# Kernel tuning notes

Hardware: AMD Instinct MI355X
Metric: run time of the kernel (lower is better)

Reference implementation:

```python
import jax, jax.numpy as jnp
import numpy as np

B, F, V, K, D, H = 16384, 26, 100000, 16, 13, 400
IN_DIM = F * K + D  # 429
EPS = 1e-5


def _bn(x, g, b):
    # BatchNorm1d in training mode: batch statistics (biased var, like torch)
    m = jnp.mean(x, axis=0)
    v = jnp.mean((x - m) ** 2, axis=0)
    return g * (x - m) / jnp.sqrt(v + EPS) + b


def setup_inputs() -> dict:
    key = jax.random.key(0)
    ks = jax.random.split(key, 12)
    X_cat = jax.random.randint(ks[0], (B, F), 0, V)
    X_dense = jax.random.normal(ks[1], (B, D), dtype=jnp.float32)
    fm1_tables = jax.random.normal(ks[2], (F, V, 1), dtype=jnp.float32) * 0.01
    emb_tables = jax.random.normal(ks[3], (F, V, K), dtype=jnp.float32) * 0.01
    Wd = jax.random.normal(ks[4], (D, 1), dtype=jnp.float32) * 0.1
    bd = jnp.zeros((1,), jnp.float32)
    W1 = jax.random.normal(ks[5], (IN_DIM, H), dtype=jnp.float32) * (1.0 / np.sqrt(IN_DIM))
    b1 = jnp.zeros((H,), jnp.float32)
    g1 = jnp.ones((H,), jnp.float32)
    be1 = jnp.zeros((H,), jnp.float32)
    W2 = jax.random.normal(ks[6], (H, H), dtype=jnp.float32) * (1.0 / np.sqrt(H))
    b2 = jnp.zeros((H,), jnp.float32)
    g2 = jnp.ones((H,), jnp.float32)
    be2 = jnp.zeros((H,), jnp.float32)
    W3 = jax.random.normal(ks[7], (H, 1), dtype=jnp.float32) * (1.0 / np.sqrt(H))
    b3 = jnp.zeros((1,), jnp.float32)
    return dict(X_cat=X_cat, X_dense=X_dense, fm1_tables=fm1_tables,
                emb_tables=emb_tables, Wd=Wd, bd=bd, W1=W1, b1=b1, g1=g1,
                be1=be1, W2=W2, b2=b2, g2=g2, be2=be2, W3=W3, b3=b3)


def reference(X_cat, X_dense, fm1_tables, emb_tables, Wd, bd,
              W1, b1, g1, be1, W2, b2, g2, be2, W3, b3):
    gather = jax.vmap(lambda tab, idx: tab[idx], in_axes=(0, 1), out_axes=1)
    # 1st order: [B, F, 1] -> sum over fields -> [B, 1]
    y_1st = jnp.sum(gather(fm1_tables, X_cat), axis=1) + X_dense @ Wd + bd
    # 2nd order embeddings: [B, F, K]
    emb = gather(emb_tables, X_cat)
    s = jnp.sum(emb, axis=1)                 # [B, K]
    ix = s ** 2 - jnp.sum(emb ** 2, axis=1)  # [B, K]
    fm_y = 0.5 * jnp.sum(ix, axis=1, keepdims=True)
    # DNN on [flattened embeddings, dense]
    x = jnp.concatenate([emb.reshape(emb.shape[0], -1), X_dense], axis=1)
    h = jax.nn.relu(_bn(x @ W1 + b1, g1, be1))
    h = jax.nn.relu(_bn(h @ W2 + b2, g2, be2))
    dnn_y = h @ W3 + b3
    return y_1st + fm_y + dnn_y
```

## Files before the change

### kernel.cpp

```cpp
#include <hip/hip_runtime.h>
#include <stdint.h>

#define B_ROWS 16384
#define NF 26
#define NV 100000
#define ND 13
#define NH 400
#define XPAD 448
#define ZPAD 416
#define EPS 1e-5f

typedef __attribute__((ext_vector_type(8))) short short8;
typedef __attribute__((ext_vector_type(4))) float f32x4;
typedef __attribute__((ext_vector_type(4))) unsigned int uint4v;

__device__ inline float bf2f(unsigned short u) {
    union { unsigned int i; float f; } v; v.i = (unsigned int)u << 16; return v.f;
}
__device__ inline unsigned short f2bf(float f) {
    union { float f; unsigned int i; } v; v.f = f;
    unsigned int r = (v.i + 0x7fff + ((v.i >> 16) & 1)) >> 16;
    return (unsigned short)r;
}

#define X_OFF    0
#define Z1_OFF   14680064
#define W1S_OFF  28311552
#define W2S_OFF  28712960
#define BASE_OFF 29085696
#define ST_OFF   29151232

__global__ __launch_bounds__(256) void gather_prep(
    const int* __restrict__ Xcat, const float* __restrict__ Xdense,
    const float* __restrict__ fm1, const float* __restrict__ emb,
    const float* __restrict__ Wd, const float* __restrict__ bd,
    const float* __restrict__ W1, const float* __restrict__ W2,
    unsigned short* __restrict__ X, float* __restrict__ base,
    unsigned short* __restrict__ W1s, unsigned short* __restrict__ W2s,
    float* __restrict__ st)
{
    int tid = threadIdx.x;
    if (blockIdx.x >= 1024) {
        int c = (blockIdx.x - 1024) * 256 + tid;
        if (c < 256) {
            for (int i = tid; i < 1664; i += 256) st[i] = 0.f;
        }
        const float* W; unsigned short* dst; int K; int cc;
        if (c < 25088) { W = W1; dst = W1s; K = 429; cc = c; }
        else           { W = W2; dst = W2s; K = 400; cc = c - 25088; }
        int n  = cc % 448;
        int q  = (cc / 448) & 3;
        int kt = cc / 1792;
        unsigned short o[8];
        #pragma unroll
        for (int j = 0; j < 8; ++j) {
            int k = kt * 32 + q * 8 + j;
            float v = (n < NH && k < K) ? W[(size_t)k * NH + n] : 0.f;
            o[j] = f2bf(v);
        }
        *(uint4v*)(dst + (size_t)cc * 8) = *(uint4v*)o;
        return;
    }
    int r = blockIdx.x * 16 + (tid >> 4);
    int k = tid & 15;
    const int* idxp = Xcat + (size_t)r * NF;
    unsigned short* xrow = X + (size_t)r * XPAD;

    float s = 0.f, ss = 0.f;
    #pragma unroll
    for (int f = 0; f < NF; ++f) {
        int idx = idxp[f];
        float v = emb[((size_t)f * NV + idx) * 16 + k];
        s += v; ss += v * v;
        xrow[f * 16 + k] = f2bf(v);
    }
    float fmsum = fm1[(size_t)k * NV + idxp[k]];
    if (k < NF - 16) fmsum += fm1[(size_t)(k + 16) * NV + idxp[k + 16]];
    float dsum = 0.f;
    if (k < ND) {
        float xd = Xdense[(size_t)r * ND + k];
        dsum = xd * Wd[k];
        xrow[NF * 16 + k] = f2bf(xd);
    }
    xrow[429 + k] = 0;
    if (k < 3) xrow[445 + k] = 0;

    float ix = s * s - ss;
    float rf = fmsum, rd = dsum;
    #pragma unroll
    for (int off = 8; off; off >>= 1) {
        ix += __shfl_xor(ix, off, 16);
        rf += __shfl_xor(rf, off, 16);
        rd += __shfl_xor(rd, off, 16);
    }
    if (k == 0) base[r] = 0.5f * ix + rf + rd + bd[0];
}

template<int NT, int LDA, bool APPLY_BN>
__global__ __launch_bounds__(512, 2) void mfma_gemm(
    const unsigned short* __restrict__ A,
    const unsigned short* __restrict__ Wst,
    const float* __restrict__ bias,
    const float* __restrict__ gsumIn, const float* __restrict__ gsqIn,
    const float* __restrict__ g, const float* __restrict__ be,
    unsigned short* __restrict__ Z, int ldz,
    float* __restrict__ gsum, float* __restrict__ gsq)
{
    __shared__ unsigned short b_s[2][1792 * 8];
    __shared__ float sredS[4][416];
    __shared__ float sredQ[4][416];
    __shared__ float alpha_s[416], beta_s[416];

    const int tid = threadIdx.x;
    const int lane = tid & 63;
    const int wv = tid >> 6;
    const int rowgrp = wv & 3;
    const int nhalf = wv >> 2;
    const int l15 = lane & 15;
    const int qh = lane >> 4;
    const int m0 = blockIdx.x * 64;
    const int arow = m0 + rowgrp * 16 + l15;
    const int c0 = nhalf * 208;
    const int NFRAG = nhalf ? 12 : 13;

    if constexpr (APPLY_BN) {
        for (int c = tid; c < ZPAD; c += 512) {
            float a = 0.f, b = 0.f;
            if (c < NH) {
                float mean = gsumIn[c] * (1.f / B_ROWS);
                float var  = gsqIn[c] * (1.f / B_ROWS) - mean * mean;
                a = g[c] * rsqrtf(var + EPS);
                b = be[c] - mean * a;
            }
            alpha_s[c] = a; beta_s[c] = b;
        }
    }

    f32x4 acc[13];
    #pragma unroll
    for (int i = 0; i < 13; ++i) acc[i] = f32x4{0.f, 0.f, 0.f, 0.f};

    uint4v rg[4];
    #pragma unroll
    for (int i = 0; i < 4; ++i) {
        int c = i * 512 + tid;
        if (c < 1792) rg[i] = *(const uint4v*)(Wst + (size_t)c * 8);
    }
    short8 af_next = *(const short8*)(A + (size_t)arow * LDA + qh * 8);

    for (int kt = 0; kt < NT; ++kt) {
        __syncthreads();
        #pragma unroll
        for (int i = 0; i < 4; ++i) {
            int c = i * 512 + tid;
            if (c < 1792) *(uint4v*)(&b_s[kt & 1][(size_t)c * 8]) = rg[i];
        }
        if (kt + 1 < NT) {
            #pragma unroll
            for (int i = 0; i < 4; ++i) {
                int c = i * 512 + tid;
                if (c < 1792)
                    rg[i] = *(const uint4v*)(Wst + (size_t)(kt + 1) * 14336 + (size_t)c * 8);
            }
        }
        short8 af = af_next;
        if (kt + 1 < NT)
            af_next = *(const short8*)(A + (size_t)arow * LDA + (kt + 1) * 32 + qh * 8);

        if constexpr (APPLY_BN) {
            const int k0 = kt * 32 + qh * 8;
            #pragma unroll
            for (int j = 0; j < 8; ++j) {
                float f = bf2f((unsigned short)af[j]);
                f = fmaxf(0.f, alpha_s[k0 + j] * f + beta_s[k0 + j]);
                af[j] = (short)f2bf(f);
            }
        }
        __syncthreads();
        const unsigned short* bb = &b_s[kt & 1][(size_t)(qh * 448 + c0 + l15) * 8];
        #pragma unroll
        for (int nn = 0; nn < 13; ++nn) {
            if (nn < NFRAG) {
                short8 bf = *(const short8*)(bb + nn * 128);
                acc[nn] = __builtin_amdgcn_mfma_f32_16x16x32_bf16(af, bf, acc[nn], 0, 0, 0);
            }
        }
    }

    #pragma unroll
    for (int nn = 0; nn < 13; ++nn) {
        if (nn < NFRAG) {
            int col = c0 + nn * 16 + l15;
            float bv = bias[col];
            float ps = 0.f, pq = 0.f;
            #pragma unroll
            for (int q = 0; q < 4; ++q) {
                float v = acc[nn][q] + bv;
                ps += v; pq += v * v;
                Z[(size_t)(m0 + rowgrp * 16 + qh * 4 + q) * ldz + col] = f2bf(v);
            }
            ps += __shfl_xor(ps, 16, 64); ps += __shfl_xor(ps, 32, 64);
            pq += __shfl_xor(pq, 16, 64); pq += __shfl_xor(pq, 32, 64);
            if (lane < 16) { sredS[rowgrp][col] = ps; sredQ[rowgrp][col] = pq; }
        }
    }
    if (nhalf == 1) {
        int col = NH + l15;
        if (col < ldz) {
            #pragma unroll
            for (int q = 0; q < 4; ++q)
                Z[(size_t)(m0 + rowgrp * 16 + qh * 4 + q) * ldz + col] = 0;
        }
    }
    __syncthreads();
    for (int c = tid; c < NH; c += 512) {
        float s = sredS[0][c] + sredS[1][c] + sredS[2][c] + sredS[3][c];
        float q = sredQ[0][c] + sredQ[1][c] + sredQ[2][c] + sredQ[3][c];
        atomicAdd(&gsum[c], s);
        atomicAdd(&gsq[c], q);
    }
}

__global__ __launch_bounds__(256) void final_kernel(
    const unsigned short* __restrict__ Z2,
    const float* __restrict__ gsum2, const float* __restrict__ gsq2,
    const float* __restrict__ g2, const float* __restrict__ be2,
    const float* __restrict__ W3, const float* __restrict__ b3,
    const float* __restrict__ base, float* __restrict__ out)
{
    __shared__ float a2s[NH], b2s[NH], w3s[NH];
    int tid = threadIdx.x;
    for (int c = tid; c < NH; c += 256) {
        float mean = gsum2[c] * (1.f / B_ROWS);
        float var  = gsq2[c] * (1.f / B_ROWS) - mean * mean;
        float a = g2[c] * rsqrtf(var + EPS);
        a2s[c] = a;
        b2s[c] = be2[c] - mean * a;
        w3s[c] = W3[c];
    }
    __syncthreads();
    int lane = tid & 63;
    int wv = tid >> 6;
    bool act = lane < 50;
    int cb = lane * 8;
    float al[8], bb[8], w3[8];
    #pragma unroll
    for (int j = 0; j < 8; ++j) {
        al[j] = act ? a2s[cb + j] : 0.f;
        bb[j] = act ? b2s[cb + j] : 0.f;
        w3[j] = act ? w3s[cb + j] : 0.f;
    }
    int r0 = blockIdx.x * 32 + wv * 8;
    float bias3 = b3[0];
    for (int t = 0; t < 8; t += 2) {
        int r = r0 + t;
        float acc0 = 0.f, acc1 = 0.f;
        if (act) {
            short8 z0 = *(const short8*)(Z2 + (size_t)r * ZPAD + cb);
            short8 z1 = *(const short8*)(Z2 + (size_t)(r + 1) * ZPAD + cb);
            #pragma unroll
            for (int j = 0; j < 8; ++j) {
                acc0 += fmaxf(0.f, al[j] * bf2f((unsigned short)z0[j]) + bb[j]) * w3[j];
                acc1 += fmaxf(0.f, al[j] * bf2f((unsigned short)z1[j]) + bb[j]) * w3[j];
            }
        }
        #pragma unroll
        for (int off = 32; off; off >>= 1) {
            acc0 += __shfl_xor(acc0, off, 64);
            acc1 += __shfl_xor(acc1, off, 64);
        }
        if (lane == 0) out[r] = base[r] + acc0 + bias3;
        if (lane == 1) out[r + 1] = base[r + 1] + acc1 + bias3;
    }
}

extern "C" void kernel_launch(void* const* d_in, const int* in_sizes, int n_in,
                              void* d_out, int out_size, void* d_ws, size_t ws_size,
                              hipStream_t stream)
{
    const int*   Xcat = (const int*)d_in[0];
    const float* Xd   = (const float*)d_in[1];
    const float* fm1  = (const float*)d_in[2];
    const float* emb  = (const float*)d_in[3];
    const float* Wd   = (const float*)d_in[4];
    const float* bd   = (const float*)d_in[5];
    const float* W1   = (const float*)d_in[6];
    const float* b1   = (const float*)d_in[7];
    const float* g1   = (const float*)d_in[8];
    const float* be1  = (const float*)d_in[9];
    const float* W2   = (const float*)d_in[10];
    const float* b2   = (const float*)d_in[11];
    const float* g2   = (const float*)d_in[12];
    const float* be2  = (const float*)d_in[13];
    const float* W3   = (const float*)d_in[14];
    const float* b3   = (const float*)d_in[15];

    char* ws = (char*)d_ws;
    unsigned short* X   = (unsigned short*)(ws + X_OFF);
    unsigned short* Z1  = (unsigned short*)(ws + Z1_OFF);
    unsigned short* Z2  = X;
    unsigned short* W1s = (unsigned short*)(ws + W1S_OFF);
    unsigned short* W2s = (unsigned short*)(ws + W2S_OFF);
    float* base = (float*)(ws + BASE_OFF);
    float* st   = (float*)(ws + ST_OFF);
    float* gsum1 = st;          float* gsq1 = st + 416;
    float* gsum2 = st + 832;    float* gsq2 = st + 1248;
    float* out = (float*)d_out;

    gather_prep<<<1213, 256, 0, stream>>>(Xcat, Xd, fm1, emb, Wd, bd, W1, W2,
                                          X, base, W1s, W2s, st);

    mfma_gemm<14, XPAD, false><<<256, 512, 0, stream>>>(
        X, W1s, b1, nullptr, nullptr, nullptr, nullptr, Z1, ZPAD, gsum1, gsq1);

    mfma_gemm<13, ZPAD, true><<<256, 512, 0, stream>>>(
        Z1, W2s, b2, gsum1, gsq1, g1, be1, Z2, ZPAD, gsum2, gsq2);

    final_kernel<<<512, 256, 0, stream>>>(Z2, gsum2, gsq2, g2, be2, W3, b3, base, out);
}
```

Before: 83.89 us.

## Fuse gather, both GEMMs and head into one cooperative persistent kernel

Replaces four kernel launches with a single cooperative kernel of 256 blocks that uses grid-wide syncs between stages. The embedding gather now feeds the first GEMM's A operand straight from global tables into registers, so the bf16 X buffer is never materialized. The FM sums are accumulated during the GEMM K-loop. The aim is to remove launch gaps and the X write/read round-trip. In exchange it adds three grid barriers and gathers with less coalescing inside the GEMM loop, which may stall the MFMA pipeline. Occupancy is also limited to 256 blocks.

Measured after the change: 165.1 us. +96.8%, slower.

```diff
diff --git a/kernel.cpp b/kernel.cpp
--- a/kernel.cpp
+++ b/kernel.cpp
@@ -1,12 +1,12 @@
 #include <hip/hip_runtime.h>
+#include <hip/hip_cooperative_groups.h>
 #include <stdint.h>
 
+namespace cg = cooperative_groups;
+
 #define B_ROWS 16384
-#define NF 26
 #define NV 100000
-#define ND 13
 #define NH 400
-#define XPAD 448
 #define ZPAD 416
 #define EPS 1e-5f
 
@@ -23,169 +23,32 @@
     return (unsigned short)r;
 }
 
-#define X_OFF    0
-#define Z1_OFF   14680064
-#define W1S_OFF  28311552
-#define W2S_OFF  28712960
-#define BASE_OFF 29085696
-#define ST_OFF   29151232
-
-__global__ __launch_bounds__(256) void gather_prep(
-    const int* __restrict__ Xcat, const float* __restrict__ Xdense,
-    const float* __restrict__ fm1, const float* __restrict__ emb,
-    const float* __restrict__ Wd, const float* __restrict__ bd,
-    const float* __restrict__ W1, const float* __restrict__ W2,
-    unsigned short* __restrict__ X, float* __restrict__ base,
-    unsigned short* __restrict__ W1s, unsigned short* __restrict__ W2s,
-    float* __restrict__ st)
+#define Z1_OFF   0
+#define Z2_OFF   13631488
+#define W1S_OFF  26738688
+#define W2S_OFF  27140096
+#define BASE_OFF 27512832
+#define ST_OFF   27578368
+
+struct SmemPool {
+    unsigned short b_s[2][14336];
+    union {
+        struct { float S[4][416]; float Q[4][416]; } red;
+        struct { int xcat[1664]; float dense[1024]; float wd[16]; } gat;
+    } u;
+    float alpha_s[416], beta_s[416];
+};
+
+__device__ __forceinline__ void gemm_epilogue(
+    SmemPool& sm, f32x4* acc, int tid, int m0,
+    const float* __restrict__ bias, unsigned short* __restrict__ Z, int ldz,
+    bool padZ, float* __restrict__ gsum, float* __restrict__ gsq)
 {
-    int tid = threadIdx.x;
-    if (blockIdx.x >= 1024) {
-        int c = (blockIdx.x - 1024) * 256 + tid;
-        if (c < 256) {
-            for (int i = tid; i < 1664; i += 256) st[i] = 0.f;
-        }
-        const float* W; unsigned short* dst; int K; int cc;
-        if (c < 25088) { W = W1; dst = W1s; K = 429; cc = c; }
-        else           { W = W2; dst = W2s; K = 400; cc = c - 25088; }
-        int n  = cc % 448;
-        int q  = (cc / 448) & 3;
-        int kt = cc / 1792;
-        unsigned short o[8];
-        #pragma unroll
-        for (int j = 0; j < 8; ++j) {
-            int k = kt * 32 + q * 8 + j;
-            float v = (n < NH && k < K) ? W[(size_t)k * NH + n] : 0.f;
-            o[j] = f2bf(v);
-        }
-        *(uint4v*)(dst + (size_t)cc * 8) = *(uint4v*)o;
-        return;
-    }
-    int r = blockIdx.x * 16 + (tid >> 4);
-    int k = tid & 15;
-    const int* idxp = Xcat + (size_t)r * NF;
-    unsigned short* xrow = X + (size_t)r * XPAD;
-
-    float s = 0.f, ss = 0.f;
-    #pragma unroll
-    for (int f = 0; f < NF; ++f) {
-        int idx = idxp[f];
-        float v = emb[((size_t)f * NV + idx) * 16 + k];
-        s += v; ss += v * v;
-        xrow[f * 16 + k] = f2bf(v);
-    }
-    float fmsum = fm1[(size_t)k * NV + idxp[k]];
-    if (k < NF - 16) fmsum += fm1[(size_t)(k + 16) * NV + idxp[k + 16]];
-    float dsum = 0.f;
-    if (k < ND) {
-        float xd = Xdense[(size_t)r * ND + k];
-        dsum = xd * Wd[k];
-        xrow[NF * 16 + k] = f2bf(xd);
-    }
-    xrow[429 + k] = 0;
-    if (k < 3) xrow[445 + k] = 0;
-
-    float ix = s * s - ss;
-    float rf = fmsum, rd = dsum;
-    #pragma unroll
-    for (int off = 8; off; off >>= 1) {
-        ix += __shfl_xor(ix, off, 16);
-        rf += __shfl_xor(rf, off, 16);
-        rd += __shfl_xor(rd, off, 16);
-    }
-    if (k == 0) base[r] = 0.5f * ix + rf + rd + bd[0];
-}
-
-template<int NT, int LDA, bool APPLY_BN>
-__global__ __launch_bounds__(512, 2) void mfma_gemm(
-    const unsigned short* __restrict__ A,
-    const unsigned short* __restrict__ Wst,
-    const float* __restrict__ bias,
-    const float* __restrict__ gsumIn, const float* __restrict__ gsqIn,
-    const float* __restrict__ g, const float* __restrict__ be,
-    unsigned short* __restrict__ Z, int ldz,
-    float* __restrict__ gsum, float* __restrict__ gsq)
-{
-    __shared__ unsigned short b_s[2][1792 * 8];
-    __shared__ float sredS[4][416];
-    __shared__ float sredQ[4][416];
-    __shared__ float alpha_s[416], beta_s[416];
-
-    const int tid = threadIdx.x;
-    const int lane = tid & 63;
-    const int wv = tid >> 6;
-    const int rowgrp = wv & 3;
-    const int nhalf = wv >> 2;
-    const int l15 = lane & 15;
-    const int qh = lane >> 4;
-    const int m0 = blockIdx.x * 64;
-    const int arow = m0 + rowgrp * 16 + l15;
+    const int lane = tid & 63, wv = tid >> 6;
+    const int rowgrp = wv & 3, nhalf = wv >> 2;
+    const int l15 = lane & 15, qh = lane >> 4;
     const int c0 = nhalf * 208;
     const int NFRAG = nhalf ? 12 : 13;
-
-    if constexpr (APPLY_BN) {
-        for (int c = tid; c < ZPAD; c += 512) {
-            float a = 0.f, b = 0.f;
-            if (c < NH) {
-                float mean = gsumIn[c] * (1.f / B_ROWS);
-                float var  = gsqIn[c] * (1.f / B_ROWS) - mean * mean;
-                a = g[c] * rsqrtf(var + EPS);
-                b = be[c] - mean * a;
-            }
-            alpha_s[c] = a; beta_s[c] = b;
-        }
-    }
-
-    f32x4 acc[13];
-    #pragma unroll
-    for (int i = 0; i < 13; ++i) acc[i] = f32x4{0.f, 0.f, 0.f, 0.f};
-
-    uint4v rg[4];
-    #pragma unroll
-    for (int i = 0; i < 4; ++i) {
-        int c = i * 512 + tid;
-        if (c < 1792) rg[i] = *(const uint4v*)(Wst + (size_t)c * 8);
-    }
-    short8 af_next = *(const short8*)(A + (size_t)arow * LDA + qh * 8);
-
-    for (int kt = 0; kt < NT; ++kt) {
-        __syncthreads();
-        #pragma unroll
-        for (int i = 0; i < 4; ++i) {
-            int c = i * 512 + tid;
-            if (c < 1792) *(uint4v*)(&b_s[kt & 1][(size_t)c * 8]) = rg[i];
-        }
-        if (kt + 1 < NT) {
-            #pragma unroll
-            for (int i = 0; i < 4; ++i) {
-                int c = i * 512 + tid;
-                if (c < 1792)
-                    rg[i] = *(const uint4v*)(Wst + (size_t)(kt + 1) * 14336 + (size_t)c * 8);
-            }
-        }
-        short8 af = af_next;
-        if (kt + 1 < NT)
-            af_next = *(const short8*)(A + (size_t)arow * LDA + (kt + 1) * 32 + qh * 8);
-
-        if constexpr (APPLY_BN) {
-            const int k0 = kt * 32 + qh * 8;
-            #pragma unroll
-            for (int j = 0; j < 8; ++j) {
-                float f = bf2f((unsigned short)af[j]);
-                f = fmaxf(0.f, alpha_s[k0 + j] * f + beta_s[k0 + j]);
-                af[j] = (short)f2bf(f);
-            }
-        }
-        __syncthreads();
-        const unsigned short* bb = &b_s[kt & 1][(size_t)(qh * 448 + c0 + l15) * 8];
-        #pragma unroll
-        for (int nn = 0; nn < 13; ++nn) {
-            if (nn < NFRAG) {
-                short8 bf = *(const short8*)(bb + nn * 128);
-                acc[nn] = __builtin_amdgcn_mfma_f32_16x16x32_bf16(af, bf, acc[nn], 0, 0, 0);
-            }
-        }
-    }
 
     #pragma unroll
     for (int nn = 0; nn < 13; ++nn) {
@@ -201,10 +64,10 @@
             }
             ps += __shfl_xor(ps, 16, 64); ps += __shfl_xor(ps, 32, 64);
             pq += __shfl_xor(pq, 16, 64); pq += __shfl_xor(pq, 32, 64);
-            if (lane < 16) { sredS[rowgrp][col] = ps; sredQ[rowgrp][col] = pq; }
-        }
-    }
-    if (nhalf == 1) {
+            if (lane < 16) { sm.u.red.S[rowgrp][col] = ps; sm.u.red.Q[rowgrp][col] = pq; }
+        }
+    }
+    if (padZ && nhalf == 1) {
         int col = NH + l15;
         if (col < ldz) {
             #pragma unroll
@@ -214,63 +77,276 @@
     }
     __syncthreads();
     for (int c = tid; c < NH; c += 512) {
-        float s = sredS[0][c] + sredS[1][c] + sredS[2][c] + sredS[3][c];
-        float q = sredQ[0][c] + sredQ[1][c] + sredQ[2][c] + sredQ[3][c];
-        atomicAdd(&gsum[c], s);
-        atomicAdd(&gsq[c], q);
-    }
-}
-
-__global__ __launch_bounds__(256) void final_kernel(
-    const unsigned short* __restrict__ Z2,
-    const float* __restrict__ gsum2, const float* __restrict__ gsq2,
+        atomicAdd(&gsum[c], sm.u.red.S[0][c] + sm.u.red.S[1][c] + sm.u.red.S[2][c] + sm.u.red.S[3][c]);
+        atomicAdd(&gsq[c],  sm.u.red.Q[0][c] + sm.u.red.Q[1][c] + sm.u.red.Q[2][c] + sm.u.red.Q[3][c]);
+    }
+}
+
+__global__ __launch_bounds__(512, 4) void deepfm_mega(
+    const int* __restrict__ Xcat, const float* __restrict__ Xd,
+    const float* __restrict__ fm1, const float* __restrict__ emb,
+    const float* __restrict__ Wd, const float* __restrict__ bd,
+    const float* __restrict__ W1, const float* __restrict__ b1,
+    const float* __restrict__ g1, const float* __restrict__ be1,
+    const float* __restrict__ W2, const float* __restrict__ b2,
     const float* __restrict__ g2, const float* __restrict__ be2,
     const float* __restrict__ W3, const float* __restrict__ b3,
-    const float* __restrict__ base, float* __restrict__ out)
+    unsigned short* __restrict__ Z1, unsigned short* __restrict__ Z2,
+    unsigned short* __restrict__ W1s, unsigned short* __restrict__ W2s,
+    float* __restrict__ base, float* __restrict__ st, float* __restrict__ out)
 {
-    __shared__ float a2s[NH], b2s[NH], w3s[NH];
-    int tid = threadIdx.x;
-    for (int c = tid; c < NH; c += 256) {
-        float mean = gsum2[c] * (1.f / B_ROWS);
-        float var  = gsq2[c] * (1.f / B_ROWS) - mean * mean;
-        float a = g2[c] * rsqrtf(var + EPS);
-        a2s[c] = a;
-        b2s[c] = be2[c] - mean * a;
-        w3s[c] = W3[c];
+    cg::grid_group grid = cg::this_grid();
+    __shared__ SmemPool sm;
+
+    const int tid = threadIdx.x;
+    const int bid = blockIdx.x;
+    const int lane = tid & 63;
+    const int wv = tid >> 6;
+    const int rowgrp = wv & 3, nhalf = wv >> 2;
+    const int l15 = lane & 15, qh = lane >> 4;
+    const int m0 = bid * 64;
+    const int rloc = rowgrp * 16 + l15;
+    const int arow = m0 + rloc;
+    const int c0 = nhalf * 208;
+    const int NFRAG = nhalf ? 12 : 13;
+
+    {
+        int c = bid * 512 + tid;
+        if (c < 48384) {
+            const float* W; unsigned short* dst; int K; int cc;
+            if (c < 25088) { W = W1; dst = W1s; K = 429; cc = c; }
+            else           { W = W2; dst = W2s; K = 400; cc = c - 25088; }
+            int n  = cc % 448;
+            int q  = (cc / 448) & 3;
+            int kt = cc / 1792;
+            unsigned short o[8];
+            #pragma unroll
+            for (int j = 0; j < 8; ++j) {
+                int k = kt * 32 + q * 8 + j;
+                float v = (n < NH && k < K) ? W[(size_t)k * NH + n] : 0.f;
+                o[j] = f2bf(v);
+            }
+            *(uint4v*)(dst + (size_t)cc * 8) = *(uint4v*)o;
+        } else if (c < 48384 + 1664) {
+            st[c - 48384] = 0.f;
+        }
+        for (int i = tid; i < 1664; i += 512)
+            sm.u.gat.xcat[i] = Xcat[(size_t)m0 * 26 + i];
+        for (int i = tid; i < 832; i += 512) {
+            int r = i / 13, cc2 = i % 13;
+            sm.u.gat.dense[r * 16 + cc2] = Xd[(size_t)m0 * 13 + i];
+        }
+        for (int i = tid; i < 192; i += 512)
+            sm.u.gat.dense[(i / 3) * 16 + 13 + (i % 3)] = 0.f;
+        if (tid < 16) sm.u.gat.wd[tid] = (tid < 13) ? Wd[tid] : 0.f;
     }
     __syncthreads();
-    int lane = tid & 63;
-    int wv = tid >> 6;
-    bool act = lane < 50;
-    int cb = lane * 8;
-    float al[8], bb[8], w3[8];
-    #pragma unroll
-    for (int j = 0; j < 8; ++j) {
-        al[j] = act ? a2s[cb + j] : 0.f;
-        bb[j] = act ? b2s[cb + j] : 0.f;
-        w3[j] = act ? w3s[cb + j] : 0.f;
-    }
-    int r0 = blockIdx.x * 32 + wv * 8;
-    float bias3 = b3[0];
-    for (int t = 0; t < 8; t += 2) {
-        int r = r0 + t;
-        float acc0 = 0.f, acc1 = 0.f;
-        if (act) {
-            short8 z0 = *(const short8*)(Z2 + (size_t)r * ZPAD + cb);
-            short8 z1 = *(const short8*)(Z2 + (size_t)(r + 1) * ZPAD + cb);
-            #pragma unroll
-            for (int j = 0; j < 8; ++j) {
-                acc0 += fmaxf(0.f, al[j] * bf2f((unsigned short)z0[j]) + bb[j]) * w3[j];
-                acc1 += fmaxf(0.f, al[j] * bf2f((unsigned short)z1[j]) + bb[j]) * w3[j];
-            }
-        }
-        #pragma unroll
-        for (int off = 32; off; off >>= 1) {
-            acc0 += __shfl_xor(acc0, off, 64);
-            acc1 += __shfl_xor(acc1, off, 64);
-        }
-        if (lane == 0) out[r] = base[r] + acc0 + bias3;
-        if (lane == 1) out[r + 1] = base[r + 1] + acc1 + bias3;
+
+    auto ld_tile = [&](int kt, float (&v)[8]) {
+        if (kt < 13) {
+            int f = 2 * kt + (qh >> 1);
+            int idx = sm.u.gat.xcat[rloc * 26 + f];
+            const float* p = emb + (((size_t)f * NV + (size_t)idx) << 4) + ((qh & 1) << 3);
+            f32x4 x0 = *(const f32x4*)p;
+            f32x4 x1 = *(const f32x4*)(p + 4);
+            v[0] = x0[0]; v[1] = x0[1]; v[2] = x0[2]; v[3] = x0[3];
+            v[4] = x1[0]; v[5] = x1[1]; v[6] = x1[2]; v[7] = x1[3];
+        } else {
+            #pragma unroll
+            for (int j = 0; j < 8; ++j)
+                v[j] = (qh < 2) ? sm.u.gat.dense[rloc * 16 + ((qh & 1) << 3) + j] : 0.f;
+        }
+    };
+
+    float va[8], vb[8];
+    ld_tile(0, va);
+    ld_tile(1, vb);
+    float fmsum = 0.f, dsum = 0.f;
+    if (nhalf == 0) {
+        for (int f = qh; f < 26; f += 4)
+            fmsum += fm1[(size_t)f * NV + sm.u.gat.xcat[rloc * 26 + f]];
+        if (qh < 2) {
+            #pragma unroll
+            for (int j = 0; j < 8; ++j)
+                dsum += sm.u.gat.dense[rloc * 16 + (qh & 1) * 8 + j] * sm.u.gat.wd[(qh & 1) * 8 + j];
+        }
+    }
+
+    grid.sync();
+
+    f32x4 acc[13];
+    #pragma unroll
+    for (int i = 0; i < 13; ++i) acc[i] = f32x4{0.f, 0.f, 0.f, 0.f};
+    uint4v rg[4];
+    #pragma unroll
+    for (int i = 0; i < 4; ++i) {
+        int c = i * 512 + tid;
+        if (c < 1792) rg[i] = *(const uint4v*)(W1s + (size_t)c * 8);
+    }
+    float s8[8] = {0.f, 0.f, 0.f, 0.f, 0.f, 0.f, 0.f, 0.f};
+    float ssacc = 0.f;
+
+    auto body1 = [&](int kt, int par, float (&v)[8]) {
+        __syncthreads();
+        #pragma unroll
+        for (int i = 0; i < 4; ++i) {
+            int c = i * 512 + tid;
+            if (c < 1792) *(uint4v*)(&sm.b_s[par][(size_t)c * 8]) = rg[i];
+        }
+        if (kt + 1 < 14) {
+            #pragma unroll
+            for (int i = 0; i < 4; ++i) {
+                int c = i * 512 + tid;
+                if (c < 1792)
+                    rg[i] = *(const uint4v*)(W1s + (size_t)(kt + 1) * 14336 + (size_t)c * 8);
+            }
+        }
+        if (kt < 13 && nhalf == 0) {
+            #pragma unroll
+            for (int j = 0; j < 8; ++j) { s8[j] += v[j]; ssacc += v[j] * v[j]; }
+        }
+        short8 af;
+        #pragma unroll
+        for (int j = 0; j < 8; ++j) af[j] = (short)f2bf(v[j]);
+        if (kt + 2 < 14) ld_tile(kt + 2, v);
+        __syncthreads();
+        const unsigned short* bb = &sm.b_s[par][(size_t)(qh * 448 + c0 + l15) * 8];
+        #pragma unroll
+        for (int nn = 0; nn < 13; ++nn) {
+            if (nn < NFRAG) {
+                short8 bf = *(const short8*)(bb + nn * 128);
+                acc[nn] = __builtin_amdgcn_mfma_f32_16x16x32_bf16(af, bf, acc[nn], 0, 0, 0);
+            }
+        }
+    };
+    for (int kt2 = 0; kt2 < 14; kt2 += 2) {
+        body1(kt2, 0, va);
+        body1(kt2 + 1, 1, vb);
+    }
+
+    if (nhalf == 0) {
+        float red = 0.f;
+        #pragma unroll
+        for (int j = 0; j < 8; ++j) {
+            float sf = s8[j] + __shfl_xor(s8[j], 32, 64);
+            red += sf * sf;
+        }
+        red -= (ssacc + __shfl_xor(ssacc, 32, 64));
+        red += __shfl_xor(red, 16, 64);
+        float fr = fmsum + __shfl_xor(fmsum, 16, 64);
+        fr += __shfl_xor(fr, 32, 64);
+        float dr = dsum + __shfl_xor(dsum, 16, 64);
+        dr += __shfl_xor(dr, 32, 64);
+        if (qh == 0) base[arow] = 0.5f * red + fr + dr + bd[0];
+    }
+    gemm_epilogue(sm, acc, tid, m0, b1, Z1, ZPAD, true, st, st + 416);
+
+    grid.sync();
+
+    {
+        const float* gs = st; const float* gq = st + 416;
+        for (int c = tid; c < ZPAD; c += 512) {
+            float a = 0.f, b = 0.f;
+            if (c < NH) {
+                float mean = gs[c] * (1.f / B_ROWS);
+                float var  = gq[c] * (1.f / B_ROWS) - mean * mean;
+                a = g1[c] * rsqrtf(var + EPS);
+                b = be1[c] - mean * a;
+            }
+            sm.alpha_s[c] = a; sm.beta_s[c] = b;
+        }
+    }
+    #pragma unroll
+    for (int i = 0; i < 13; ++i) acc[i] = f32x4{0.f, 0.f, 0.f, 0.f};
+    #pragma unroll
+    for (int i = 0; i < 4; ++i) {
+        int c = i * 512 + tid;
+        if (c < 1792) rg[i] = *(const uint4v*)(W2s + (size_t)c * 8);
+    }
+    short8 af_next = *(const short8*)(Z1 + (size_t)arow * ZPAD + qh * 8);
+
+    for (int kt = 0; kt < 13; ++kt) {
+        __syncthreads();
+        #pragma unroll
+        for (int i = 0; i < 4; ++i) {
+            int c = i * 512 + tid;
+            if (c < 1792) *(uint4v*)(&sm.b_s[kt & 1][(size_t)c * 8]) = rg[i];
+        }
+        if (kt + 1 < 13) {
+            #pragma unroll
+            for (int i = 0; i < 4; ++i) {
+                int c = i * 512 + tid;
+                if (c < 1792)
+                    rg[i] = *(const uint4v*)(W2s + (size_t)(kt + 1) * 14336 + (size_t)c * 8);
+            }
+        }
+        short8 af = af_next;
+        if (kt + 1 < 13)
+            af_next = *(const short8*)(Z1 + (size_t)arow * ZPAD + (kt + 1) * 32 + qh * 8);
+        int k0 = kt * 32 + qh * 8;
+        #pragma unroll
+        for (int j = 0; j < 8; ++j) {
+            float f = bf2f((unsigned short)af[j]);
+            f = fmaxf(0.f, sm.alpha_s[k0 + j] * f + sm.beta_s[k0 + j]);
+            af[j] = (short)f2bf(f);
+        }
+        __syncthreads();
+        const unsigned short* bb = &sm.b_s[kt & 1][(size_t)(qh * 448 + c0 + l15) * 8];
+        #pragma unroll
+        for (int nn = 0; nn < 13; ++nn) {
+            if (nn < NFRAG) {
+                short8 bf = *(const short8*)(bb + nn * 128);
+                acc[nn] = __builtin_amdgcn_mfma_f32_16x16x32_bf16(af, bf, acc[nn], 0, 0, 0);
+            }
+        }
+    }
+    gemm_epilogue(sm, acc, tid, m0, b2, Z2, 400, false, st + 832, st + 1248);
+
+    grid.sync();
+
+    {
+        const float* gs = st + 832; const float* gq = st + 1248;
+        float* w3s = sm.u.red.S[0];
+        for (int c = tid; c < NH; c += 512) {
+            float mean = gs[c] * (1.f / B_ROWS);
+            float var  = gq[c] * (1.f / B_ROWS) - mean * mean;
+            float a = g2[c] * rsqrtf(var + EPS);
+            sm.alpha_s[c] = a;
+            sm.beta_s[c]  = be2[c] - mean * a;
+            w3s[c] = W3[c];
+        }
+        __syncthreads();
+        bool act2 = lane < 50;
+        int cb = lane * 8;
+        float al[8], bbv[8], w3[8];
+        #pragma unroll
+        for (int j = 0; j < 8; ++j) {
+            al[j]  = act2 ? sm.alpha_s[cb + j] : 0.f;
+            bbv[j] = act2 ? sm.beta_s[cb + j] : 0.f;
+            w3[j]  = act2 ? w3s[cb + j] : 0.f;
+        }
+        int r0 = m0 + wv * 8;
+        float bias3 = b3[0];
+        for (int t = 0; t < 8; t += 2) {
+            int r = r0 + t;
+            float a0 = 0.f, a1 = 0.f;
+            if (act2) {
+                short8 z0 = *(const short8*)(Z2 + (size_t)r * 400 + cb);
+                short8 z1 = *(const short8*)(Z2 + (size_t)(r + 1) * 400 + cb);
+                #pragma unroll
+                for (int j = 0; j < 8; ++j) {
+                    a0 += fmaxf(0.f, al[j] * bf2f((unsigned short)z0[j]) + bbv[j]) * w3[j];
+                    a1 += fmaxf(0.f, al[j] * bf2f((unsigned short)z1[j]) + bbv[j]) * w3[j];
+                }
+            }
+            #pragma unroll
+            for (int off = 32; off; off >>= 1) {
+                a0 += __shfl_xor(a0, off, 64);
+                a1 += __shfl_xor(a1, off, 64);
+            }
+            if (lane == 0) out[r] = base[r] + a0 + bias3;
+            if (lane == 1) out[r + 1] = base[r + 1] + a1 + bias3;
+        }
     }
 }
 
@@ -296,25 +372,21 @@
     const float* b3   = (const float*)d_in[15];
 
     char* ws = (char*)d_ws;
-    unsigned short* X   = (unsigned short*)(ws + X_OFF);
     unsigned short* Z1  = (unsigned short*)(ws + Z1_OFF);
-    unsigned short* Z2  = X;
+    unsigned short* Z2  = (unsigned short*)(ws + Z2_OFF);
     unsigned short* W1s = (unsigned short*)(ws + W1S_OFF);
     unsigned short* W2s = (unsigned short*)(ws + W2S_OFF);
     float* base = (float*)(ws + BASE_OFF);
     float* st   = (float*)(ws + ST_OFF);
-    float* gsum1 = st;          float* gsq1 = st + 416;
-    float* gsum2 = st + 832;    float* gsq2 = st + 1248;
-    float* out = (float*)d_out;
-
-    gather_prep<<<1213, 256, 0, stream>>>(Xcat, Xd, fm1, emb, Wd, bd, W1, W2,
-                                          X, base, W1s, W2s, st);
-
-    mfma_gemm<14, XPAD, false><<<256, 512, 0, stream>>>(
-        X, W1s, b1, nullptr, nullptr, nullptr, nullptr, Z1, ZPAD, gsum1, gsq1);
-
-    mfma_gemm<13, ZPAD, true><<<256, 512, 0, stream>>>(
-        Z1, W2s, b2, gsum1, gsq1, g1, be1, Z2, ZPAD, gsum2, gsq2);
-
-    final_kernel<<<512, 256, 0, stream>>>(Z2, gsum2, gsq2, g2, be2, W3, b3, base, out);
-}
+    float* out  = (float*)d_out;
+
+    void* args[] = {
+        (void*)&Xcat, (void*)&Xd, (void*)&fm1, (void*)&emb,
+        (void*)&Wd, (void*)&bd, (void*)&W1, (void*)&b1, (void*)&g1, (void*)&be1,
+        (void*)&W2, (void*)&b2, (void*)&g2, (void*)&be2, (void*)&W3, (void*)&b3,
+        (void*)&Z1, (void*)&Z2, (void*)&W1s, (void*)&W2s,
+        (void*)&base, (void*)&st, (void*)&out
+    };
+    hipLaunchCooperativeKernel((const void*)deepfm_mega, dim3(256), dim3(512),
+                               args, 0, stream);
+}
```
